# Optimization experiments

Measured on AMD Instinct MI355X. Metric: run time of the kernel, lower is better.

## Reference

```python
import jax, jax.numpy as jnp
import numpy as np

N, D = 16384, 256

def setup_inputs() -> dict:
    key = jax.random.key(0)
    k1, k2 = jax.random.split(key)
    image_emb = jax.random.normal(k1, (N, D), dtype=jnp.float32)
    text_emb = jax.random.normal(k2, (N, D), dtype=jnp.float32)
    return {"image_emb": image_emb, "text_emb": text_emb}

def reference(image_emb, text_emb):
    n = image_emb.shape[0]
    # [n, n] similarity logits
    logits = image_emb @ text_emb.T
    labels = jnp.arange(n)
    # cross-entropy with diagonal labels: -log_softmax(logits)[i, i]
    logp_t = jax.nn.log_softmax(logits, axis=-1)        # image -> text (rows)
    logp_i = jax.nn.log_softmax(logits.T, axis=-1)      # text -> image (cols)
    loss_t = -logp_t[labels, labels]
    loss_i = -logp_i[labels, labels]
    loss = ((loss_i + loss_t) * 0.5).mean()
    return loss
```

## Files before the change

kernel.cpp:

```cpp
#include <hip/hip_runtime.h>
#include <hip/hip_bf16.h>

#define NN 16384
#define DD 256

typedef unsigned short u16;
typedef unsigned int u32;
typedef unsigned char u8;
typedef long i64;
typedef __attribute__((ext_vector_type(4))) float f32x4;
typedef __attribute__((ext_vector_type(4))) int i32x4;
typedef __attribute__((ext_vector_type(8))) int i32x8;

static __device__ __forceinline__ void gload16(const u8* g, u8* l) {
    __builtin_amdgcn_global_load_lds(
        (const __attribute__((address_space(1))) void*)g,
        (__attribute__((address_space(3))) void*)l,
        16, 0, 0);
}

__global__ void prep_kernel(const float* __restrict__ img, const float* __restrict__ txt,
                            u8* __restrict__ A8, u8* __restrict__ B8,
                            float* __restrict__ zbuf ,
                            float* __restrict__ out) {
    int gid = blockIdx.x * 256 + threadIdx.x;
    float4 va = ((const float4*)img)[gid];
    float4 vb = ((const float4*)txt)[gid];
    const float S = 1.44269504088896f;
    int pa = __builtin_amdgcn_cvt_pk_fp8_f32(va.x * S, va.y * S, 0, false);
    pa     = __builtin_amdgcn_cvt_pk_fp8_f32(va.z * S, va.w * S, pa, true);
    int pb = __builtin_amdgcn_cvt_pk_fp8_f32(vb.x, vb.y, 0, false);
    pb     = __builtin_amdgcn_cvt_pk_fp8_f32(vb.z, vb.w, pb, true);

    const int r  = gid >> 6;
    const int rl = r & 127;
    const int pn = r >> 7;
    const int ko = (gid & 63) << 2;
    const int kbA = ko ^ ((rl & 15) << 3);
    *(u32*)(A8 + ((size_t)pn << 15) + (rl << 8) + kbA) = (u32)pa;
    const int mm  = rl & 15, cb8 = rl >> 4;
    const int k2  = ko >> 7, koo = ko & 127;
    const int qq  = koo >> 5, jj = (koo >> 4) & 1, u = ko & 15;
    *(u32*)(B8 + ((size_t)pn << 15) + (k2 << 14) + (cb8 << 11) + (jj << 10)
               + (qq << 8) + (mm << 4) + u) = (u32)pb;
    if (gid < 32768) zbuf[gid] = 0.0f;
    if (gid == 0) out[0] = 0.0f;
}

__global__ __launch_bounds__(256, 2) void gemm_lse_kernel(
        const u8* __restrict__ A8, const u8* __restrict__ B8,
        float* __restrict__ s_row, float* __restrict__ s_col,
        float* __restrict__ diag) {
    __shared__ u8 sA[32768];

    const int t = threadIdx.x;
    const int lane = t & 63;
    const int w = t >> 6;
    const int wr = w >> 1, wc = w & 1;
    const int q = lane >> 4, m = lane & 15;
    const int bi = blockIdx.x & 127;
    const int jg = blockIdx.x >> 7;
    const int row0 = bi << 7;

    #pragma unroll
    for (int R = 0; R < 8; ++R)
        gload16(A8 + ((size_t)bi << 15) + (R << 12) + (w << 10) + ((size_t)lane << 4),
                &sA[(R << 12) + (w << 10)]);
    __syncthreads();

    i32x8 areg[2][4];
    #pragma unroll
    for (int k2 = 0; k2 < 2; ++k2)
        #pragma unroll
        for (int rb = 0; rb < 4; ++rb) {
            const int rr = (wr << 6) + (rb << 4) + m;
            union { i32x8 v; i64 d[4]; } ua;
            #pragma unroll
            for (int j = 0; j < 4; ++j)
                ua.d[j] = *(const i64*)(&sA[(rr << 8) + (k2 << 7)
                           + (((q << 5) | (j << 3)) ^ (m << 3))]);
            areg[k2][rb] = ua.v;
        }

    const f32x4 fzero = {0.f, 0.f, 0.f, 0.f};
    const f32x4 cinit = {-144.f, -144.f, -144.f, -144.f};
    f32x4 acc[4][4];
    f32x4 rp[4] = {fzero, fzero, fzero, fzero};

    const u8* Bw = B8 + (wc << 13) + ((size_t)lane << 4);

    i32x8 bfA[4], bfB[4];

    {
        const int ct0 = (jg << 4) | (bi & 15);
        const u8* p = Bw + ((size_t)ct0 << 15);
        #pragma unroll
        for (int cb = 0; cb < 4; ++cb) {
            i32x4 lo = *(const i32x4*)(p + (cb << 11));
            i32x4 hi = *(const i32x4*)(p + (cb << 11) + 1024);
            bfA[cb] = __builtin_shufflevector(lo, hi, 0, 1, 2, 3, 4, 5, 6, 7);
        }
    }

    #pragma unroll 1
    for (int jt = 0; jt < 16; ++jt) {
        const int ct = (jg << 4) | ((jt + bi) & 15);
        const int col0 = ct << 7;
        const u8* p = Bw + ((size_t)ct << 15);

        #pragma unroll
        for (int cb = 0; cb < 4; ++cb) {
            i32x4 lo = *(const i32x4*)(p + 16384 + (cb << 11));
            i32x4 hi = *(const i32x4*)(p + 16384 + (cb << 11) + 1024);
            bfB[cb] = __builtin_shufflevector(lo, hi, 0, 1, 2, 3, 4, 5, 6, 7);
        }

        __builtin_amdgcn_s_setprio(1);
        #pragma unroll
        for (int rb = 0; rb < 4; ++rb)
            #pragma unroll
            for (int cb = 0; cb < 4; ++cb)
                acc[rb][cb] = __builtin_amdgcn_mfma_scale_f32_16x16x128_f8f6f4(
                    areg[0][rb], bfA[cb], cinit, 0, 0, 0, 127, 0, 127);
        __builtin_amdgcn_s_setprio(0);

        if (jt < 15) {
            const int ctn = (jg << 4) | ((jt + 1 + bi) & 15);
            const u8* pn2 = Bw + ((size_t)ctn << 15);
            #pragma unroll
            for (int cb = 0; cb < 4; ++cb) {
                i32x4 lo = *(const i32x4*)(pn2 + (cb << 11));
                i32x4 hi = *(const i32x4*)(pn2 + (cb << 11) + 1024);
                bfA[cb] = __builtin_shufflevector(lo, hi, 0, 1, 2, 3, 4, 5, 6, 7);
            }
        }

        __builtin_amdgcn_s_setprio(1);
        #pragma unroll
        for (int rb = 0; rb < 4; ++rb)
            #pragma unroll
            for (int cb = 0; cb < 4; ++cb)
                acc[rb][cb] = __builtin_amdgcn_mfma_scale_f32_16x16x128_f8f6f4(
                    areg[1][rb], bfB[cb], acc[rb][cb], 0, 0, 0, 127, 0, 127);
        __builtin_amdgcn_s_setprio(0);

        if (bi == ct && wr == wc) {
            #pragma unroll
            for (int rb = 0; rb < 4; ++rb)
                #pragma unroll
                for (int r = 0; r < 4; ++r)
                    if (m == ((q << 2) | r))
                        diag[row0 + (wr << 6) + (rb << 4) + m] = acc[rb][rb][r];
        }
        #pragma unroll
        for (int rb = 0; rb < 4; ++rb)
            #pragma unroll
            for (int cb = 0; cb < 4; ++cb)
                #pragma unroll
                for (int r = 0; r < 4; ++r)
                    acc[rb][cb][r] = __builtin_amdgcn_exp2f(acc[rb][cb][r]);

        #pragma unroll
        for (int rb = 0; rb < 4; ++rb)
            rp[rb] += (acc[rb][0] + acc[rb][1]) + (acc[rb][2] + acc[rb][3]);

        float cpart = 0.0f;
        #pragma unroll
        for (int cb = 0; cb < 4; ++cb) {
            float v = 0.0f;
            #pragma unroll
            for (int rb = 0; rb < 4; ++rb)
                v += (acc[rb][cb][0] + acc[rb][cb][1]) + (acc[rb][cb][2] + acc[rb][cb][3]);
            v += __shfl_xor(v, 16, 64);
            v += __shfl_xor(v, 32, 64);
            if (q == cb) cpart = v;
        }
        atomicAdd(&s_col[col0 + (wc << 6) + (q << 4) + m], cpart);
    }

    float rout = 0.0f;
    #pragma unroll
    for (int rb = 0; rb < 4; ++rb)
        #pragma unroll
        for (int r = 0; r < 4; ++r) {
            float v = rp[rb][r];
            v += __shfl_xor(v, 1, 16);
            v += __shfl_xor(v, 2, 16);
            v += __shfl_xor(v, 4, 16);
            v += __shfl_xor(v, 8, 16);
            if (m == ((rb << 2) | r)) rout = v;
        }
    atomicAdd(&s_row[row0 + (wr << 6) + ((m >> 2) << 4) + (q << 2) + (m & 3)], rout);
}

__global__ void final_kernel(const float* __restrict__ s_row, const float* __restrict__ s_col,
                             const float* __restrict__ diag, float* __restrict__ out) {
    __shared__ double red[256];
    int t = threadIdx.x;
    int i = blockIdx.x * 256 + t;
    double p = 0.5 * (double)(log2f(s_row[i]) + log2f(s_col[i])) - (double)diag[i];
    red[t] = p;
    __syncthreads();
    for (int s = 128; s > 0; s >>= 1) {
        if (t < s) red[t] += red[t + s];
        __syncthreads();
    }
    if (t == 0) atomicAdd(out, (float)(red[0] * 0.6931471805599453 / (double)NN));
}

extern "C" void kernel_launch(void* const* d_in, const int* in_sizes, int n_in,
                              void* d_out, int out_size, void* d_ws, size_t ws_size,
                              hipStream_t stream) {
    const float* img = (const float*)d_in[0];
    const float* txt = (const float*)d_in[1];
    char* ws = (char*)d_ws;
    u8*    A8    = (u8*)ws;
    u8*    B8    = (u8*)(ws + 4194304);
    float* s_row = (float*)(ws + 8388608);
    float* s_col = (float*)(ws + 8388608 + 65536);
    float* diag  = (float*)(ws + 8388608 + 131072);
    float* out   = (float*)d_out;

    prep_kernel<<<4096, 256, 0, stream>>>(img, txt, A8, B8, s_row, out);
    gemm_lse_kernel<<<1024, 256, 0, stream>>>(A8, B8, s_row, s_col, diag);
    final_kernel<<<64, 256, 0, stream>>>(s_row, s_col, diag, out);
}
```

Before: 151.0 us.

## Store A in MFMA fragment layout and load operands directly from global

The prep kernel now stages each 16-row chunk of both inputs in padded shared memory and writes A and B in the same fragment-ready layout, using coalesced 16-byte stores instead of scattered 4-byte stores. The GEMM kernel drops its shared-memory staging of A and the swizzled LDS reads, loading A fragments straight from global memory as it already does for B. This removes the LDS traffic and a barrier from the main kernel and may let more blocks fit per CU. In exchange prep uses a grid four times smaller with extra shared-memory work.

```diff
diff --git a/kernel.cpp b/kernel.cpp
--- a/kernel.cpp
+++ b/kernel.cpp
@@ -12,37 +12,41 @@
 typedef __attribute__((ext_vector_type(4))) int i32x4;
 typedef __attribute__((ext_vector_type(8))) int i32x8;
 
-static __device__ __forceinline__ void gload16(const u8* g, u8* l) {
-    __builtin_amdgcn_global_load_lds(
-        (const __attribute__((address_space(1))) void*)g,
-        (__attribute__((address_space(3))) void*)l,
-        16, 0, 0);
-}
-
-__global__ void prep_kernel(const float* __restrict__ img, const float* __restrict__ txt,
-                            u8* __restrict__ A8, u8* __restrict__ B8,
-                            float* __restrict__ zbuf ,
-                            float* __restrict__ out) {
-    int gid = blockIdx.x * 256 + threadIdx.x;
-    float4 va = ((const float4*)img)[gid];
-    float4 vb = ((const float4*)txt)[gid];
+__global__ __launch_bounds__(256) void prep_kernel(
+        const float* __restrict__ img, const float* __restrict__ txt,
+        u8* __restrict__ A8, u8* __restrict__ B8,
+        float* __restrict__ zbuf ,
+        float* __restrict__ out) {
+    __shared__ u32 sA[16 * 65 + 8];
+    __shared__ u32 sB[16 * 65 + 8];
+    const int t = threadIdx.x, bi = blockIdx.x;
+    const float4* ib = (const float4*)img + ((size_t)bi << 10);
+    const float4* tb = (const float4*)txt + ((size_t)bi << 10);
     const float S = 1.44269504088896f;
-    int pa = __builtin_amdgcn_cvt_pk_fp8_f32(va.x * S, va.y * S, 0, false);
-    pa     = __builtin_amdgcn_cvt_pk_fp8_f32(va.z * S, va.w * S, pa, true);
-    int pb = __builtin_amdgcn_cvt_pk_fp8_f32(vb.x, vb.y, 0, false);
-    pb     = __builtin_amdgcn_cvt_pk_fp8_f32(vb.z, vb.w, pb, true);
-
-    const int r  = gid >> 6;
-    const int rl = r & 127;
-    const int pn = r >> 7;
-    const int ko = (gid & 63) << 2;
-    const int kbA = ko ^ ((rl & 15) << 3);
-    *(u32*)(A8 + ((size_t)pn << 15) + (rl << 8) + kbA) = (u32)pa;
-    const int mm  = rl & 15, cb8 = rl >> 4;
-    const int k2  = ko >> 7, koo = ko & 127;
-    const int qq  = koo >> 5, jj = (koo >> 4) & 1, u = ko & 15;
-    *(u32*)(B8 + ((size_t)pn << 15) + (k2 << 14) + (cb8 << 11) + (jj << 10)
-               + (qq << 8) + (mm << 4) + u) = (u32)pb;
+    #pragma unroll
+    for (int k = 0; k < 4; ++k) {
+        const int idx = (k << 8) + t;
+        const int row = idx >> 6, col = idx & 63;
+        float4 va = ib[idx];
+        int pa = __builtin_amdgcn_cvt_pk_fp8_f32(va.x * S, va.y * S, 0, false);
+        pa     = __builtin_amdgcn_cvt_pk_fp8_f32(va.z * S, va.w * S, pa, true);
+        sA[row * 65 + col] = (u32)pa;
+        float4 vb = tb[idx];
+        int pb = __builtin_amdgcn_cvt_pk_fp8_f32(vb.x, vb.y, 0, false);
+        pb     = __builtin_amdgcn_cvt_pk_fp8_f32(vb.z, vb.w, pb, true);
+        sB[row * 65 + col] = (u32)pb;
+    }
+    __syncthreads();
+    const int w = t >> 6, l = t & 63;
+    const int k2 = w >> 1, jj = w & 1, qq = l >> 4, mm = l & 15;
+    const int wb = mm * 65 + (k2 << 5) + (qq << 3) + (jj << 2);
+    i32x4 oa = { (int)sA[wb], (int)sA[wb + 1], (int)sA[wb + 2], (int)sA[wb + 3] };
+    i32x4 ob = { (int)sB[wb], (int)sB[wb + 1], (int)sB[wb + 2], (int)sB[wb + 3] };
+    const size_t dst = ((size_t)(bi >> 3) << 15) + (k2 << 14) + ((size_t)(bi & 7) << 11)
+                     + (jj << 10) + (qq << 8) + (mm << 4);
+    *(i32x4*)(A8 + dst) = oa;
+    *(i32x4*)(B8 + dst) = ob;
+    const int gid = (bi << 8) + t;
     if (gid < 32768) zbuf[gid] = 0.0f;
     if (gid == 0) out[0] = 0.0f;
 }
@@ -51,8 +55,6 @@
         const u8* __restrict__ A8, const u8* __restrict__ B8,
         float* __restrict__ s_row, float* __restrict__ s_col,
         float* __restrict__ diag) {
-    __shared__ u8 sA[32768];
-
     const int t = threadIdx.x;
     const int lane = t & 63;
     const int w = t >> 6;
@@ -62,24 +64,16 @@
     const int jg = blockIdx.x >> 7;
     const int row0 = bi << 7;
 
-    #pragma unroll
-    for (int R = 0; R < 8; ++R)
-        gload16(A8 + ((size_t)bi << 15) + (R << 12) + (w << 10) + ((size_t)lane << 4),
-                &sA[(R << 12) + (w << 10)]);
-    __syncthreads();
-
+    const u8* Aw = A8 + ((size_t)bi << 15) + ((size_t)lane << 4);
     i32x8 areg[2][4];
     #pragma unroll
     for (int k2 = 0; k2 < 2; ++k2)
         #pragma unroll
         for (int rb = 0; rb < 4; ++rb) {
-            const int rr = (wr << 6) + (rb << 4) + m;
-            union { i32x8 v; i64 d[4]; } ua;
-            #pragma unroll
-            for (int j = 0; j < 4; ++j)
-                ua.d[j] = *(const i64*)(&sA[(rr << 8) + (k2 << 7)
-                           + (((q << 5) | (j << 3)) ^ (m << 3))]);
-            areg[k2][rb] = ua.v;
+            const u8* p = Aw + (k2 << 14) + (((wr << 2) + rb) << 11);
+            i32x4 lo = *(const i32x4*)(p);
+            i32x4 hi = *(const i32x4*)(p + 1024);
+            areg[k2][rb] = __builtin_shufflevector(lo, hi, 0, 1, 2, 3, 4, 5, 6, 7);
         }
 
     const f32x4 fzero = {0.f, 0.f, 0.f, 0.f};
@@ -221,7 +215,7 @@
     float* diag  = (float*)(ws + 8388608 + 131072);
     float* out   = (float*)d_out;
 
-    prep_kernel<<<4096, 256, 0, stream>>>(img, txt, A8, B8, s_row, out);
+    prep_kernel<<<1024, 256, 0, stream>>>(img, txt, A8, B8, s_row, out);
     gemm_lse_kernel<<<1024, 256, 0, stream>>>(A8, B8, s_row, s_col, diag);
     final_kernel<<<64, 256, 0, stream>>>(s_row, s_col, diag, out);
 }
```

Result: no change. 150.2 us (-0.5%).
